# Optimization experiments

Hardware: AMD Instinct MI355X
Metric: run time of the kernel (lower is better)

## Reference

```python
import jax, jax.numpy as jnp
import numpy as np

C = 2.0 + 1e-6
_nodes, _weights = np.polynomial.laguerre.laggauss(2)
QUAD_NODES = jnp.asarray(np.maximum(_nodes, 0.01) / C, dtype=jnp.float32)
QUAD_WEIGHTS = jnp.asarray(np.maximum(_weights, 0.01) / C, dtype=jnp.float32)
H, HD, P, M = 4, 64, 16, 32  # heads, head_dim, poly_dim, num_features
NUM_LABELS = 131072


def safe_normalize(x, axis=-1, eps=1e-4):
    n = jnp.linalg.norm(x, axis=axis, keepdims=True)
    return x / jnp.maximum(n, eps)


def safe_log(x, eps=1e-8):
    return jnp.log(jnp.maximum(x, eps))


def slay_features(x, omega, anchors):
    # x: [N, H*HD]; omega: [R,H,HD,M] (pre-scaled); anchors: [P,HD] (unit-norm)
    N = x.shape[0]
    xr = safe_normalize(x.reshape(N, H, HD), axis=-1)
    poly_proj = jnp.clip(jnp.einsum('nhd,pd->nhp', xr, anchors), -1.0, 1.0)
    poly_feat = poly_proj ** 2 / np.float32(np.sqrt(P))          # [N,H,P]
    prf_proj = jnp.einsum('nhd,rhdm->rnhm', xr, omega)           # [R,N,H,M]
    s = jnp.maximum(QUAD_NODES, 1e-6).reshape(-1, 1, 1, 1)
    exp_arg = jnp.clip(prf_proj * jnp.sqrt(2.0 * s) - s, -20.0, 20.0)
    prf_feat = jnp.exp(exp_arg) / np.float32(np.sqrt(M + 1e-6))
    prf_feat = prf_feat * jnp.sqrt(jnp.maximum(QUAD_WEIGHTS, 1e-6)).reshape(-1, 1, 1, 1)
    # fuse poly x prf, concat over quadrature nodes r (r-major feature order)
    fused = poly_feat[None, :, :, :, None] * prf_feat[:, :, :, None, :]  # [R,N,H,P,M]
    return fused.transpose(1, 0, 2, 3, 4).reshape(N, -1)         # [N, R*H*P*M]


def setup_inputs() -> dict:
    key = jax.random.key(0)
    ks = jax.random.split(key, 9)
    B, L, K = 1024, 128, 8
    return {
        'indices': jax.random.randint(ks[0], (B, L), 0, 100000),
        'mask': jnp.ones((B, L), dtype=jnp.float32),
        'labels': jax.random.randint(ks[1], (B, K), 0, NUM_LABELS),
        'label_mask': jnp.ones((B, K), dtype=jnp.float32),
        'neg_indices': jax.random.randint(ks[2], (2048,), 0, NUM_LABELS),
        'embed_table': jax.random.normal(ks[3], (100000, 256), dtype=jnp.float32),
        'kernel': jax.random.normal(ks[4], (256, NUM_LABELS), dtype=jnp.float32),
        'omega': jax.random.normal(ks[5], (2, H, HD, M), dtype=jnp.float32),
        'anchors': jax.random.normal(ks[6], (P, HD), dtype=jnp.float32),
    }


def reference(indices, mask, labels, label_mask, neg_indices, embed_table, kernel, omega, anchors):
    B, K = labels.shape
    # init-time parameter normalizations from the module
    omega_n = omega / np.float32(np.sqrt(HD))
    anchors_n = anchors / jnp.linalg.norm(anchors, axis=-1, keepdims=True)
    # MeanEmbedding encoder
    embeds = embed_table[indices]                                 # [B,L,D]
    summed = jnp.sum(embeds * mask[:, :, None], axis=1)
    query = summed / jnp.maximum(jnp.sum(mask, axis=1, keepdims=True), 1.0)
    query = safe_normalize(query, axis=-1)
    phi_query = slay_features(query, omega_n, anchors_n)          # [B,F]
    # sampled classifier rows
    W = safe_normalize(kernel.T, axis=-1)                         # [num_labels,D]
    safe_labels = jnp.maximum(labels, 0)
    all_needed = jnp.concatenate([safe_labels.reshape(-1), neg_indices])  # [B*K+Nneg]
    W_subset = W[all_needed]
    phi_W = slay_features(W_subset, omega_n, anchors_n)           # [B*K+Nneg,F]
    scores = phi_query @ phi_W.T                                  # [B, B*K+Nneg]
    idx_offsets = jnp.arange(B)[:, None] * K + jnp.arange(K)[None, :]
    pos_scores = jnp.take_along_axis(scores, idx_offsets, axis=1) # [B,K]
    neg_scores = scores[:, B * K:]                                # [B,Nneg]
    all_scores = jnp.concatenate([pos_scores, neg_scores], axis=1) + 1e-8
    log_Z = jax.scipy.special.logsumexp(safe_log(all_scores), axis=1)
    log_probs = safe_log(pos_scores + 1e-8) - log_Z[:, None]
    return -jnp.sum(log_probs * label_mask) / (jnp.sum(label_mask) + 1e-6)
```

## Files before the change

kernel.cpp:

```cpp
#include <hip/hip_runtime.h>
#include <math.h>

#define B_Q 1024
#define L_SEQ 128
#define D_EMB 256
#define NLAB 131072
#define LBL_ROWS 8192
#define NEG_ROWS 2048
#define W_ROWS 10240
#define CROW 320
#define LST 82
#define RPB 8

__device__ __forceinline__ float wave_sum(float v) {
#pragma unroll
  for (int off = 32; off > 0; off >>= 1) v += __shfl_xor(v, off, 64);
  return v;
}

__device__ __forceinline__ void slay_tail(const float* __restrict__ sx, int t,
                                          const float* __restrict__ anchT,
                                          const float* __restrict__ omega,
                                          float* __restrict__ outrow) {
  if (t < 64) {
    const int h = t >> 4, p = t & 15;
    const float* x = sx + h * 64;
    float d = 0.f;
#pragma unroll
    for (int dd = 0; dd < 64; dd++) d = fmaf(x[dd], anchT[dd * 16 + p], d);
    d = fminf(fmaxf(d, -1.0f), 1.0f);
    outrow[h * 16 + p] = d * d * 0.25f;
  }
  {
    const int r = t >> 7, h = (t >> 5) & 3;
    const float* x = sx + h * 64;
    const float* om = omega + (size_t)(t >> 5) * 2048 + (t & 31);
    float d = 0.f;
#pragma unroll
    for (int dd = 0; dd < 64; dd++) d = fmaf(x[dd], om[dd * 32], d);
    const float proj = d * 0.125f;
    const float s = r ? 1.70710592763316f : 0.29289307236691f;
    const float w = r ? 0.07322326809171f : 0.42677648190829f;
    float arg = proj * sqrtf(2.0f * s) - s;
    arg = fminf(fmaxf(arg, -20.0f), 20.0f);
    outrow[64 + t] = expf(arg) * (sqrtf(w) / sqrtf(32.000001f));
  }
}

__global__ __launch_bounds__(256) void k_prep(const float* __restrict__ anchors,
                                              float* __restrict__ anchT,
                                              float* __restrict__ negparts,
                                              int* __restrict__ hist) {
  const int t = threadIdx.x, bx = blockIdx.x;
  if (bx == 0) {
    if (t < 64) {
      for (int p = 0; p < 16; p++) {
        const float v = anchors[p * 64 + t];
        const float n = sqrtf(wave_sum(v * v));
        anchT[t * 16 + p] = v / n;
      }
    }
  } else if (bx <= 256) {
    negparts[(bx - 1) * 256 + t] = 0.f;
  } else {
    hist[(bx - 257) * 256 + t] = 0;
  }
}

__global__ __launch_bounds__(256) void k_mark(const int* __restrict__ labels,
                                              const int* __restrict__ negidx,
                                              int* __restrict__ jidx,
                                              int* __restrict__ hist) {
  const int i = blockIdx.x * 256 + threadIdx.x;
  if (i >= W_ROWS) return;
  int j;
  if (i < LBL_ROWS) { j = labels[i]; if (j < 0) j = 0; }
  else               { j = negidx[i - LBL_ROWS]; }
  jidx[i] = j;
  atomicAdd(&hist[j >> 6], 1);
}

__global__ __launch_bounds__(256) void k_scan(int* __restrict__ hist) {
  __shared__ int s[256];
  const int t = threadIdx.x;
  int v[8]; int sum = 0;
#pragma unroll
  for (int e = 0; e < 8; e++) { v[e] = hist[t * 8 + e]; sum += v[e]; }
  s[t] = sum; __syncthreads();
  for (int off = 1; off < 256; off <<= 1) {
    const int x = s[t];
    const int y = (t >= off) ? s[t - off] : 0;
    __syncthreads();
    s[t] = x + y;
    __syncthreads();
  }
  int run = s[t] - sum;
#pragma unroll
  for (int e = 0; e < 8; e++) { hist[t * 8 + e] = run; run += v[e]; }
}

__global__ __launch_bounds__(256) void k_scatter(const int* __restrict__ jidx,
                                                 int* __restrict__ hist,
                                                 int* __restrict__ sorted) {
  const int i = blockIdx.x * 256 + threadIdx.x;
  if (i >= W_ROWS) return;
  const int pos = atomicAdd(&hist[jidx[i] >> 6], 1);
  sorted[pos] = i;
}

__global__ __launch_bounds__(256) void k_query(const int* __restrict__ indices,
                                               const float* __restrict__ mask,
                                               const float* __restrict__ embed,
                                               const float* __restrict__ anchT,
                                               const float* __restrict__ omega,
                                               float* __restrict__ qcomp) {
  const int b = blockIdx.x, t = threadIdx.x;
  const int wv = t >> 6, ln = t & 63;
  __shared__ int sidx[L_SEQ];
  __shared__ float smask[L_SEQ];
  __shared__ float4 spart[256];
  __shared__ float smsum[4];
  __shared__ float sx[256];
  if (t < L_SEQ) { sidx[t] = indices[b * L_SEQ + t]; smask[t] = mask[b * L_SEQ + t]; }
  __syncthreads();
  float4 acc = {0.f, 0.f, 0.f, 0.f};
  float msum = 0.f;
#pragma unroll 8
  for (int l = wv * 32; l < wv * 32 + 32; l++) {
    const float m = smask[l];
    msum += m;
    const float4 e = *(const float4*)(embed + (size_t)sidx[l] * D_EMB + ln * 4);
    acc.x = fmaf(e.x, m, acc.x); acc.y = fmaf(e.y, m, acc.y);
    acc.z = fmaf(e.z, m, acc.z); acc.w = fmaf(e.w, m, acc.w);
  }
  spart[wv * 64 + ln] = acc;
  if (ln == 0) smsum[wv] = msum;
  __syncthreads();
  const float* spf = (const float*)spart;
  float q = spf[t] + spf[256 + t] + spf[512 + t] + spf[768 + t];
  const float mt = smsum[0] + smsum[1] + smsum[2] + smsum[3];
  q /= fmaxf(mt, 1.0f);
  const float ss = wave_sum(q * q);
  sx[t] = q / fmaxf(sqrtf(ss), 1e-4f);
  __syncthreads();
  slay_tail(sx, t, anchT, omega, qcomp + (size_t)b * CROW);
}

__global__ __launch_bounds__(256) void k_wrows(const int* __restrict__ sorted,
                                               const int* __restrict__ jidx,
                                               const float* __restrict__ kern,
                                               const float* __restrict__ anchT,
                                               const float* __restrict__ omega,
                                               float* __restrict__ wcomp) {
  __shared__ int sj[RPB];
  __shared__ int ssid[RPB];
  __shared__ float sx[RPB * 256];
  __shared__ float snorm[RPB * 4];
  const int tid = threadIdx.x;
  const int cb = (blockIdx.x & 7) * 160 + (blockIdx.x >> 3);
  const int i0 = cb * RPB;

  if (tid < RPB) {
    const int sid = sorted[i0 + tid];
    ssid[tid] = sid;
    sj[tid] = jidx[sid];
  }
  __syncthreads();

#pragma unroll
  for (int k = 0; k < RPB; k++) {
    const int idx = k * 256 + tid;
    sx[idx] = kern[(size_t)(idx & 255) * NLAB + sj[idx >> 8]];
  }
  __syncthreads();

  {
    const int row = tid >> 5, sub = tid & 31;
    const float* xp = sx + row * 256 + sub * 8;
    float ssum = 0.f;
#pragma unroll
    for (int e = 0; e < 8; e++) ssum = fmaf(xp[e], xp[e], ssum);
    ssum += __shfl_xor(ssum, 1, 64);
    ssum += __shfl_xor(ssum, 2, 64);
    ssum += __shfl_xor(ssum, 4, 64);
    if ((sub & 7) == 0) snorm[row * 4 + (sub >> 3)] = fmaxf(sqrtf(ssum), 1e-4f);
  }
  __syncthreads();
#pragma unroll
  for (int k = 0; k < RPB; k++) {
    const int idx = k * 256 + tid;
    sx[idx] /= snorm[(idx >> 8) * 4 + ((idx >> 6) & 3)];
  }
  __syncthreads();

  {
    const int h = (tid >> 5) & 3, r = tid >> 7;
    const float* om = omega + (size_t)(tid >> 5) * 2048 + (tid & 31);
    float acc[RPB];
#pragma unroll
    for (int row = 0; row < RPB; row++) acc[row] = 0.f;
#pragma unroll
    for (int dd = 0; dd < 64; dd += 2) {
      const float o0 = om[dd * 32], o1 = om[dd * 32 + 32];
#pragma unroll
      for (int row = 0; row < RPB; row++) {
        const float2 xv = *(const float2*)(sx + row * 256 + h * 64 + dd);
        acc[row] = fmaf(xv.x, o0, fmaf(xv.y, o1, acc[row]));
      }
    }
    const float s = r ? 1.70710592763316f : 0.29289307236691f;
    const float w = r ? 0.07322326809171f : 0.42677648190829f;
    const float sc = sqrtf(2.0f * s);
    const float outs = sqrtf(w) / sqrtf(32.000001f);
#pragma unroll
    for (int row = 0; row < RPB; row++) {
      float arg = acc[row] * 0.125f * sc - s;
      arg = fminf(fmaxf(arg, -20.0f), 20.0f);
      wcomp[(size_t)ssid[row] * CROW + 64 + tid] = expf(arg) * outs;
    }
  }

  {
    const int hp = tid & 63, rp = tid >> 6;
    const int h = hp >> 4, p = hp & 15;
    const float* x0 = sx + (rp * 2) * 256 + h * 64;
    const float* x1 = x0 + 256;
    float d0 = 0.f, d1 = 0.f;
#pragma unroll
    for (int dd = 0; dd < 64; dd++) {
      const float a = anchT[dd * 16 + p];
      d0 = fmaf(x0[dd], a, d0);
      d1 = fmaf(x1[dd], a, d1);
    }
    d0 = fminf(fmaxf(d0, -1.0f), 1.0f);
    d1 = fminf(fmaxf(d1, -1.0f), 1.0f);
    wcomp[(size_t)ssid[rp * 2] * CROW + h * 16 + p]     = d0 * d0 * 0.25f;
    wcomp[(size_t)ssid[rp * 2 + 1] * CROW + h * 16 + p] = d1 * d1 * 0.25f;
  }
}

__global__ __launch_bounds__(128) void k_neg(const float* __restrict__ qcomp,
                                             const float* __restrict__ wcomp,
                                             float* __restrict__ negparts) {
  __shared__ float qt[64 * LST];
  __shared__ float wt[32 * LST];
  const int tid = threadIdx.x;
  const int qb0 = blockIdx.x * 64;
  const int wr0 = LBL_ROWS + blockIdx.y * 32;
  const int h = blockIdx.z;

  for (int idx = tid; idx < 96 * 20; idx += 128) {
    const int row = idx / 20, c4 = idx % 20;
    int col, lcol;
    if (c4 < 4)       { col = h * 16 + c4 * 4;              lcol = c4 * 4; }
    else if (c4 < 12) { col = 64 + h * 32 + (c4 - 4) * 4;   lcol = 16 + (c4 - 4) * 4; }
    else              { col = 192 + h * 32 + (c4 - 12) * 4; lcol = 48 + (c4 - 12) * 4; }
    const bool isq = row < 64;
    const int grow = isq ? (qb0 + row) : (wr0 + row - 64);
    const float4 v = *(const float4*)((isq ? qcomp : wcomp) + (size_t)grow * CROW + col);
    float* dst = (isq ? qt + row * LST : wt + (row - 64) * LST) + lcol;
    dst[0] = v.x; dst[1] = v.y; dst[2] = v.z; dst[3] = v.w;
  }
  __syncthreads();

  const int qg = tid >> 3;
  const int wg = tid & 7;
  const float* qb = qt + (qg * 4) * LST;
  const float* wb = wt + (wg * 4) * LST;

  float pd[4][4] = {{0.f}}, pf[4][4] = {{0.f}};
#pragma unroll
  for (int kc = 0; kc < 8; kc++) {
    float2 qv[4], wv[4];
#pragma unroll
    for (int i = 0; i < 4; i++) qv[i] = *(const float2*)(qb + i * LST + 2 * kc);
#pragma unroll
    for (int j = 0; j < 4; j++) wv[j] = *(const float2*)(wb + j * LST + 2 * kc);
#pragma unroll
    for (int i = 0; i < 4; i++)
#pragma unroll
      for (int j = 0; j < 4; j++) {
        pd[i][j] = fmaf(qv[i].x, wv[j].x, pd[i][j]);
        pd[i][j] = fmaf(qv[i].y, wv[j].y, pd[i][j]);
      }
  }
#pragma unroll 8
  for (int kc = 0; kc < 32; kc++) {
    float2 qv[4], wv[4];
#pragma unroll
    for (int i = 0; i < 4; i++) qv[i] = *(const float2*)(qb + i * LST + 16 + 2 * kc);
#pragma unroll
    for (int j = 0; j < 4; j++) wv[j] = *(const float2*)(wb + j * LST + 16 + 2 * kc);
#pragma unroll
    for (int i = 0; i < 4; i++)
#pragma unroll
      for (int j = 0; j < 4; j++) {
        pf[i][j] = fmaf(qv[i].x, wv[j].x, pf[i][j]);
        pf[i][j] = fmaf(qv[i].y, wv[j].y, pf[i][j]);
      }
  }

#pragma unroll
  for (int i = 0; i < 4; i++) {
    float acc = 0.f;
#pragma unroll
    for (int j = 0; j < 4; j++) acc += pd[i][j] * pf[i][j];
#pragma unroll
    for (int off = 1; off < 8; off <<= 1) acc += __shfl_xor(acc, off, 64);
    if (wg == 0) atomicAdd(&negparts[blockIdx.y * B_Q + qb0 + qg * 4 + i], acc);
  }
}

__global__ __launch_bounds__(256) void k_pos(const float* __restrict__ qcomp,
                                             const float* __restrict__ wcomp,
                                             float* __restrict__ pos) {
  const int tid = threadIdx.x;
  const int g = blockIdx.x * 64 + (tid >> 2);
  const int h = tid & 3;
  const float* q = qcomp + (size_t)(g >> 3) * CROW;
  const float* w = wcomp + (size_t)g * CROW;
  float pd = 0.f, pf = 0.f;
#pragma unroll
  for (int c = 0; c < 4; c++) {
    const float4 qv = *(const float4*)(q + h * 16 + c * 4);
    const float4 wv = *(const float4*)(w + h * 16 + c * 4);
    pd += qv.x * wv.x + qv.y * wv.y + qv.z * wv.z + qv.w * wv.w;
  }
#pragma unroll
  for (int r = 0; r < 2; r++)
#pragma unroll
    for (int c = 0; c < 8; c++) {
      const float4 qv = *(const float4*)(q + 64 + r * 128 + h * 32 + c * 4);
      const float4 wv = *(const float4*)(w + 64 + r * 128 + h * 32 + c * 4);
      pf += qv.x * wv.x + qv.y * wv.y + qv.z * wv.z + qv.w * wv.w;
    }
  float sc = pd * pf;
  sc += __shfl_xor(sc, 1, 64);
  sc += __shfl_xor(sc, 2, 64);
  if (h == 0) pos[g] = sc;
}

__global__ __launch_bounds__(1024) void k_loss(const float* __restrict__ pos,
                                               const float* __restrict__ negparts,
                                               const float* __restrict__ lmask,
                                               float* __restrict__ out) {
  const int b = threadIdx.x;
  float lp[8];
  float possum = 0.f;
#pragma unroll
  for (int k = 0; k < 8; k++) { lp[k] = pos[b * 8 + k]; possum += lp[k]; }
  float negsum = 0.f;
#pragma unroll 8
  for (int c = 0; c < 64; c++) negsum += negparts[c * B_Q + b];
  const float Z = possum + negsum + 2.056e-5f;
  const float logZ = logf(Z);
  float local = 0.f, lsum = 0.f;
#pragma unroll
  for (int k = 0; k < 8; k++) {
    const float lm = lmask[b * 8 + k];
    local += lm * (logf(lp[k] + 1e-8f) - logZ);
    lsum += lm;
  }
  local = wave_sum(local);
  lsum = wave_sum(lsum);
  __shared__ float r1[16], r2[16];
  const int wid = b >> 6;
  if ((b & 63) == 0) { r1[wid] = local; r2[wid] = lsum; }
  __syncthreads();
  if (b == 0) {
    float t1 = 0.f, t2 = 0.f;
    for (int wv = 0; wv < 16; wv++) { t1 += r1[wv]; t2 += r2[wv]; }
    out[0] = -t1 / (t2 + 1e-6f);
  }
}

extern "C" void kernel_launch(void* const* d_in, const int* in_sizes, int n_in,
                              void* d_out, int out_size, void* d_ws, size_t ws_size,
                              hipStream_t stream) {
  const int* indices  = (const int*)d_in[0];
  const float* mask   = (const float*)d_in[1];
  const int* labels   = (const int*)d_in[2];
  const float* lmask  = (const float*)d_in[3];
  const int* negidx   = (const int*)d_in[4];
  const float* embed  = (const float*)d_in[5];
  const float* kern   = (const float*)d_in[6];
  const float* omega  = (const float*)d_in[7];
  const float* anchors= (const float*)d_in[8];
  float* out = (float*)d_out;

  float* ws = (float*)d_ws;
  float* anchT    = ws;
  float* qcomp    = anchT + 1024;
  float* wcomp    = qcomp + (size_t)B_Q * CROW;
  float* pos      = wcomp + (size_t)W_ROWS * CROW;
  float* negparts = pos + LBL_ROWS;
  int*   jidx     = (int*)(negparts + 64 * B_Q);
  int*   sorted   = jidx + W_ROWS;
  int*   hist     = sorted + W_ROWS;

  k_prep<<<265, 256, 0, stream>>>(anchors, anchT, negparts, hist);
  k_mark<<<40, 256, 0, stream>>>(labels, negidx, jidx, hist);
  k_scan<<<1, 256, 0, stream>>>(hist);
  k_scatter<<<40, 256, 0, stream>>>(jidx, hist, sorted);
  k_query<<<B_Q, 256, 0, stream>>>(indices, mask, embed, anchT, omega, qcomp);
  k_wrows<<<W_ROWS / RPB, 256, 0, stream>>>(sorted, jidx, kern, anchT, omega, wcomp);
  k_neg<<<dim3(16, 64, 4), 128, 0, stream>>>(qcomp, wcomp, negparts);
  k_pos<<<128, 256, 0, stream>>>(qcomp, wcomp, pos);
  k_loss<<<1, 1024, 0, stream>>>(pos, negparts, lmask, out);
}
```

Baseline: 357.6 us.

## Fuse nine launches into four: single-block sort, merged feature and score kernels

Combines the anchor prep, histogram marking, scan and scatter into one setup kernel. The histogram work is done in shared memory by a single block instead of global atomics spread over three launches. The query-feature and W-row feature kernels become one grid split by block index, and the negative and positive scoring kernels likewise share one launch. The aim is to cut launch gaps and let independent stages overlap on the GPU. In exchange the whole sort runs serially in one block, and both fused kernels now take the larger shared-memory footprint of the two paths.

```diff
diff --git a/kernel.cpp b/kernel.cpp
--- a/kernel.cpp
+++ b/kernel.cpp
@@ -32,7 +32,8 @@
     outrow[h * 16 + p] = d * d * 0.25f;
   }
   {
-    const int r = t >> 7, h = (t >> 5) & 3;
+    const int r = t >> 7;
+    const int h = (t >> 5) & 3;
     const float* x = sx + h * 64;
     const float* om = omega + (size_t)(t >> 5) * 2048 + (t & 31);
     float d = 0.f;
@@ -47,10 +48,15 @@
   }
 }
 
-__global__ __launch_bounds__(256) void k_prep(const float* __restrict__ anchors,
-                                              float* __restrict__ anchT,
-                                              float* __restrict__ negparts,
-                                              int* __restrict__ hist) {
+__global__ __launch_bounds__(256) void k_setup(const float* __restrict__ anchors,
+                                               const int* __restrict__ labels,
+                                               const int* __restrict__ negidx,
+                                               float* __restrict__ anchT,
+                                               float* __restrict__ negparts,
+                                               int* __restrict__ jidx,
+                                               int* __restrict__ sorted) {
+  __shared__ int shist[2048];
+  __shared__ int s2[256];
   const int t = threadIdx.x, bx = blockIdx.x;
   if (bx == 0) {
     if (t < 64) {
@@ -63,281 +69,270 @@
   } else if (bx <= 256) {
     negparts[(bx - 1) * 256 + t] = 0.f;
   } else {
-    hist[(bx - 257) * 256 + t] = 0;
-  }
-}
-
-__global__ __launch_bounds__(256) void k_mark(const int* __restrict__ labels,
-                                              const int* __restrict__ negidx,
-                                              int* __restrict__ jidx,
-                                              int* __restrict__ hist) {
-  const int i = blockIdx.x * 256 + threadIdx.x;
-  if (i >= W_ROWS) return;
-  int j;
-  if (i < LBL_ROWS) { j = labels[i]; if (j < 0) j = 0; }
-  else               { j = negidx[i - LBL_ROWS]; }
-  jidx[i] = j;
-  atomicAdd(&hist[j >> 6], 1);
-}
-
-__global__ __launch_bounds__(256) void k_scan(int* __restrict__ hist) {
-  __shared__ int s[256];
-  const int t = threadIdx.x;
-  int v[8]; int sum = 0;
-#pragma unroll
-  for (int e = 0; e < 8; e++) { v[e] = hist[t * 8 + e]; sum += v[e]; }
-  s[t] = sum; __syncthreads();
-  for (int off = 1; off < 256; off <<= 1) {
-    const int x = s[t];
-    const int y = (t >= off) ? s[t - off] : 0;
-    __syncthreads();
-    s[t] = x + y;
-    __syncthreads();
-  }
-  int run = s[t] - sum;
-#pragma unroll
-  for (int e = 0; e < 8; e++) { hist[t * 8 + e] = run; run += v[e]; }
-}
-
-__global__ __launch_bounds__(256) void k_scatter(const int* __restrict__ jidx,
-                                                 int* __restrict__ hist,
-                                                 int* __restrict__ sorted) {
-  const int i = blockIdx.x * 256 + threadIdx.x;
-  if (i >= W_ROWS) return;
-  const int pos = atomicAdd(&hist[jidx[i] >> 6], 1);
-  sorted[pos] = i;
-}
-
-__global__ __launch_bounds__(256) void k_query(const int* __restrict__ indices,
-                                               const float* __restrict__ mask,
-                                               const float* __restrict__ embed,
-                                               const float* __restrict__ anchT,
-                                               const float* __restrict__ omega,
-                                               float* __restrict__ qcomp) {
-  const int b = blockIdx.x, t = threadIdx.x;
-  const int wv = t >> 6, ln = t & 63;
-  __shared__ int sidx[L_SEQ];
-  __shared__ float smask[L_SEQ];
-  __shared__ float4 spart[256];
-  __shared__ float smsum[4];
-  __shared__ float sx[256];
-  if (t < L_SEQ) { sidx[t] = indices[b * L_SEQ + t]; smask[t] = mask[b * L_SEQ + t]; }
-  __syncthreads();
-  float4 acc = {0.f, 0.f, 0.f, 0.f};
-  float msum = 0.f;
+    for (int i = t; i < 2048; i += 256) shist[i] = 0;
+    __syncthreads();
+    for (int i = t; i < W_ROWS; i += 256) {
+      int j;
+      if (i < LBL_ROWS) { j = labels[i]; if (j < 0) j = 0; }
+      else               { j = negidx[i - LBL_ROWS]; }
+      jidx[i] = j;
+      atomicAdd(&shist[j >> 6], 1);
+    }
+    __syncthreads();
+    int v[8]; int sum = 0;
+#pragma unroll
+    for (int e = 0; e < 8; e++) { v[e] = shist[t * 8 + e]; sum += v[e]; }
+    s2[t] = sum; __syncthreads();
+    for (int off = 1; off < 256; off <<= 1) {
+      const int x = s2[t];
+      const int y = (t >= off) ? s2[t - off] : 0;
+      __syncthreads();
+      s2[t] = x + y;
+      __syncthreads();
+    }
+    int run = s2[t] - sum;
+#pragma unroll
+    for (int e = 0; e < 8; e++) { shist[t * 8 + e] = run; run += v[e]; }
+    __syncthreads();
+    for (int i = t; i < W_ROWS; i += 256) {
+      const int p = atomicAdd(&shist[jidx[i] >> 6], 1);
+      sorted[p] = i;
+    }
+  }
+}
+
+__global__ __launch_bounds__(256) void k_feat(const int* __restrict__ indices,
+                                              const float* __restrict__ mask,
+                                              const float* __restrict__ embed,
+                                              const float* __restrict__ kern,
+                                              const float* __restrict__ anchT,
+                                              const float* __restrict__ omega,
+                                              const int* __restrict__ jidx,
+                                              const int* __restrict__ sorted,
+                                              float* __restrict__ qcomp,
+                                              float* __restrict__ wcomp) {
+  __shared__ __align__(16) float smem[2112];
+  const int tid = threadIdx.x;
+
+  if (blockIdx.x < B_Q) {
+    const int b = blockIdx.x, t = tid;
+    const int wv = t >> 6, ln = t & 63;
+    int* sidx = (int*)smem;
+    float* smask = smem + 128;
+    float4* spart = (float4*)(smem + 256);
+    float* smsum = smem + 1280;
+    float* sx = smem + 1296;
+    if (t < L_SEQ) { sidx[t] = indices[b * L_SEQ + t]; smask[t] = mask[b * L_SEQ + t]; }
+    __syncthreads();
+    float4 acc = {0.f, 0.f, 0.f, 0.f};
+    float msum = 0.f;
 #pragma unroll 8
-  for (int l = wv * 32; l < wv * 32 + 32; l++) {
-    const float m = smask[l];
-    msum += m;
-    const float4 e = *(const float4*)(embed + (size_t)sidx[l] * D_EMB + ln * 4);
-    acc.x = fmaf(e.x, m, acc.x); acc.y = fmaf(e.y, m, acc.y);
-    acc.z = fmaf(e.z, m, acc.z); acc.w = fmaf(e.w, m, acc.w);
-  }
-  spart[wv * 64 + ln] = acc;
-  if (ln == 0) smsum[wv] = msum;
-  __syncthreads();
-  const float* spf = (const float*)spart;
-  float q = spf[t] + spf[256 + t] + spf[512 + t] + spf[768 + t];
-  const float mt = smsum[0] + smsum[1] + smsum[2] + smsum[3];
-  q /= fmaxf(mt, 1.0f);
-  const float ss = wave_sum(q * q);
-  sx[t] = q / fmaxf(sqrtf(ss), 1e-4f);
-  __syncthreads();
-  slay_tail(sx, t, anchT, omega, qcomp + (size_t)b * CROW);
-}
-
-__global__ __launch_bounds__(256) void k_wrows(const int* __restrict__ sorted,
-                                               const int* __restrict__ jidx,
-                                               const float* __restrict__ kern,
-                                               const float* __restrict__ anchT,
-                                               const float* __restrict__ omega,
-                                               float* __restrict__ wcomp) {
-  __shared__ int sj[RPB];
-  __shared__ int ssid[RPB];
-  __shared__ float sx[RPB * 256];
-  __shared__ float snorm[RPB * 4];
-  const int tid = threadIdx.x;
-  const int cb = (blockIdx.x & 7) * 160 + (blockIdx.x >> 3);
-  const int i0 = cb * RPB;
-
-  if (tid < RPB) {
-    const int sid = sorted[i0 + tid];
-    ssid[tid] = sid;
-    sj[tid] = jidx[sid];
-  }
-  __syncthreads();
-
-#pragma unroll
-  for (int k = 0; k < RPB; k++) {
-    const int idx = k * 256 + tid;
-    sx[idx] = kern[(size_t)(idx & 255) * NLAB + sj[idx >> 8]];
-  }
-  __syncthreads();
-
-  {
-    const int row = tid >> 5, sub = tid & 31;
-    const float* xp = sx + row * 256 + sub * 8;
-    float ssum = 0.f;
-#pragma unroll
-    for (int e = 0; e < 8; e++) ssum = fmaf(xp[e], xp[e], ssum);
-    ssum += __shfl_xor(ssum, 1, 64);
-    ssum += __shfl_xor(ssum, 2, 64);
-    ssum += __shfl_xor(ssum, 4, 64);
-    if ((sub & 7) == 0) snorm[row * 4 + (sub >> 3)] = fmaxf(sqrtf(ssum), 1e-4f);
-  }
-  __syncthreads();
-#pragma unroll
-  for (int k = 0; k < RPB; k++) {
-    const int idx = k * 256 + tid;
-    sx[idx] /= snorm[(idx >> 8) * 4 + ((idx >> 6) & 3)];
-  }
-  __syncthreads();
-
-  {
-    const int h = (tid >> 5) & 3, r = tid >> 7;
-    const float* om = omega + (size_t)(tid >> 5) * 2048 + (tid & 31);
-    float acc[RPB];
-#pragma unroll
-    for (int row = 0; row < RPB; row++) acc[row] = 0.f;
-#pragma unroll
-    for (int dd = 0; dd < 64; dd += 2) {
-      const float o0 = om[dd * 32], o1 = om[dd * 32 + 32];
+    for (int l = wv * 32; l < wv * 32 + 32; l++) {
+      const float m = smask[l];
+      msum += m;
+      const float4 e = *(const float4*)(embed + (size_t)sidx[l] * D_EMB + ln * 4);
+      acc.x = fmaf(e.x, m, acc.x); acc.y = fmaf(e.y, m, acc.y);
+      acc.z = fmaf(e.z, m, acc.z); acc.w = fmaf(e.w, m, acc.w);
+    }
+    spart[wv * 64 + ln] = acc;
+    if (ln == 0) smsum[wv] = msum;
+    __syncthreads();
+    const float* spf = (const float*)spart;
+    float q = spf[t] + spf[256 + t] + spf[512 + t] + spf[768 + t];
+    const float mt = smsum[0] + smsum[1] + smsum[2] + smsum[3];
+    q /= fmaxf(mt, 1.0f);
+    const float ss = wave_sum(q * q);
+    sx[t] = q / fmaxf(sqrtf(ss), 1e-4f);
+    __syncthreads();
+    slay_tail(sx, t, anchT, omega, qcomp + (size_t)b * CROW);
+  } else {
+    const int lb = blockIdx.x - B_Q;
+    int* sj = (int*)smem;
+    int* ssid = (int*)smem + 8;
+    float* snorm = smem + 16;
+    float* sx = smem + 48;
+    const int cb = (lb & 7) * 160 + (lb >> 3);
+    const int i0 = cb * RPB;
+
+    if (tid < RPB) {
+      const int sid = sorted[i0 + tid];
+      ssid[tid] = sid;
+      sj[tid] = jidx[sid];
+    }
+    __syncthreads();
+
+#pragma unroll
+    for (int k = 0; k < RPB; k++) {
+      const int idx = k * 256 + tid;
+      sx[idx] = kern[(size_t)(idx & 255) * NLAB + sj[idx >> 8]];
+    }
+    __syncthreads();
+
+    {
+      const int row = tid >> 5, sub = tid & 31;
+      const float* xp = sx + row * 256 + sub * 8;
+      float ssum = 0.f;
+#pragma unroll
+      for (int e = 0; e < 8; e++) ssum = fmaf(xp[e], xp[e], ssum);
+      ssum += __shfl_xor(ssum, 1, 64);
+      ssum += __shfl_xor(ssum, 2, 64);
+      ssum += __shfl_xor(ssum, 4, 64);
+      if ((sub & 7) == 0) snorm[row * 4 + (sub >> 3)] = fmaxf(sqrtf(ssum), 1e-4f);
+    }
+    __syncthreads();
+#pragma unroll
+    for (int k = 0; k < RPB; k++) {
+      const int idx = k * 256 + tid;
+      sx[idx] /= snorm[(idx >> 8) * 4 + ((idx >> 6) & 3)];
+    }
+    __syncthreads();
+
+    {
+      const int h = (tid >> 5) & 3, r = tid >> 7;
+      const float* om = omega + (size_t)(tid >> 5) * 2048 + (tid & 31);
+      float acc[RPB];
+#pragma unroll
+      for (int row = 0; row < RPB; row++) acc[row] = 0.f;
+#pragma unroll
+      for (int dd = 0; dd < 64; dd += 2) {
+        const float o0 = om[dd * 32], o1 = om[dd * 32 + 32];
+#pragma unroll
+        for (int row = 0; row < RPB; row++) {
+          const float2 xv = *(const float2*)(sx + row * 256 + h * 64 + dd);
+          acc[row] = fmaf(xv.x, o0, fmaf(xv.y, o1, acc[row]));
+        }
+      }
+      const float s = r ? 1.70710592763316f : 0.29289307236691f;
+      const float w = r ? 0.07322326809171f : 0.42677648190829f;
+      const float sc = sqrtf(2.0f * s);
+      const float outs = sqrtf(w) / sqrtf(32.000001f);
 #pragma unroll
       for (int row = 0; row < RPB; row++) {
-        const float2 xv = *(const float2*)(sx + row * 256 + h * 64 + dd);
-        acc[row] = fmaf(xv.x, o0, fmaf(xv.y, o1, acc[row]));
+        float arg = acc[row] * 0.125f * sc - s;
+        arg = fminf(fmaxf(arg, -20.0f), 20.0f);
+        wcomp[(size_t)ssid[row] * CROW + 64 + tid] = expf(arg) * outs;
       }
     }
-    const float s = r ? 1.70710592763316f : 0.29289307236691f;
-    const float w = r ? 0.07322326809171f : 0.42677648190829f;
-    const float sc = sqrtf(2.0f * s);
-    const float outs = sqrtf(w) / sqrtf(32.000001f);
-#pragma unroll
-    for (int row = 0; row < RPB; row++) {
-      float arg = acc[row] * 0.125f * sc - s;
-      arg = fminf(fmaxf(arg, -20.0f), 20.0f);
-      wcomp[(size_t)ssid[row] * CROW + 64 + tid] = expf(arg) * outs;
-    }
-  }
-
-  {
-    const int hp = tid & 63, rp = tid >> 6;
-    const int h = hp >> 4, p = hp & 15;
-    const float* x0 = sx + (rp * 2) * 256 + h * 64;
-    const float* x1 = x0 + 256;
-    float d0 = 0.f, d1 = 0.f;
-#pragma unroll
-    for (int dd = 0; dd < 64; dd++) {
-      const float a = anchT[dd * 16 + p];
-      d0 = fmaf(x0[dd], a, d0);
-      d1 = fmaf(x1[dd], a, d1);
-    }
-    d0 = fminf(fmaxf(d0, -1.0f), 1.0f);
-    d1 = fminf(fmaxf(d1, -1.0f), 1.0f);
-    wcomp[(size_t)ssid[rp * 2] * CROW + h * 16 + p]     = d0 * d0 * 0.25f;
-    wcomp[(size_t)ssid[rp * 2 + 1] * CROW + h * 16 + p] = d1 * d1 * 0.25f;
-  }
-}
-
-__global__ __launch_bounds__(128) void k_neg(const float* __restrict__ qcomp,
-                                             const float* __restrict__ wcomp,
-                                             float* __restrict__ negparts) {
+
+    {
+      const int hp = tid & 63, rp = tid >> 6;
+      const int h = hp >> 4, p = hp & 15;
+      const float* x0 = sx + (rp * 2) * 256 + h * 64;
+      const float* x1 = x0 + 256;
+      float d0 = 0.f, d1 = 0.f;
+#pragma unroll
+      for (int dd = 0; dd < 64; dd++) {
+        const float a = anchT[dd * 16 + p];
+        d0 = fmaf(x0[dd], a, d0);
+        d1 = fmaf(x1[dd], a, d1);
+      }
+      d0 = fminf(fmaxf(d0, -1.0f), 1.0f);
+      d1 = fminf(fmaxf(d1, -1.0f), 1.0f);
+      wcomp[(size_t)ssid[rp * 2] * CROW + h * 16 + p]     = d0 * d0 * 0.25f;
+      wcomp[(size_t)ssid[rp * 2 + 1] * CROW + h * 16 + p] = d1 * d1 * 0.25f;
+    }
+  }
+}
+
+__global__ __launch_bounds__(128) void k_score(const float* __restrict__ qcomp,
+                                               const float* __restrict__ wcomp,
+                                               float* __restrict__ negparts,
+                                               float* __restrict__ pos) {
   __shared__ float qt[64 * LST];
   __shared__ float wt[32 * LST];
   const int tid = threadIdx.x;
-  const int qb0 = blockIdx.x * 64;
-  const int wr0 = LBL_ROWS + blockIdx.y * 32;
-  const int h = blockIdx.z;
-
-  for (int idx = tid; idx < 96 * 20; idx += 128) {
-    const int row = idx / 20, c4 = idx % 20;
-    int col, lcol;
-    if (c4 < 4)       { col = h * 16 + c4 * 4;              lcol = c4 * 4; }
-    else if (c4 < 12) { col = 64 + h * 32 + (c4 - 4) * 4;   lcol = 16 + (c4 - 4) * 4; }
-    else              { col = 192 + h * 32 + (c4 - 12) * 4; lcol = 48 + (c4 - 12) * 4; }
-    const bool isq = row < 64;
-    const int grow = isq ? (qb0 + row) : (wr0 + row - 64);
-    const float4 v = *(const float4*)((isq ? qcomp : wcomp) + (size_t)grow * CROW + col);
-    float* dst = (isq ? qt + row * LST : wt + (row - 64) * LST) + lcol;
-    dst[0] = v.x; dst[1] = v.y; dst[2] = v.z; dst[3] = v.w;
-  }
-  __syncthreads();
-
-  const int qg = tid >> 3;
-  const int wg = tid & 7;
-  const float* qb = qt + (qg * 4) * LST;
-  const float* wb = wt + (wg * 4) * LST;
-
-  float pd[4][4] = {{0.f}}, pf[4][4] = {{0.f}};
-#pragma unroll
-  for (int kc = 0; kc < 8; kc++) {
-    float2 qv[4], wv[4];
-#pragma unroll
-    for (int i = 0; i < 4; i++) qv[i] = *(const float2*)(qb + i * LST + 2 * kc);
-#pragma unroll
-    for (int j = 0; j < 4; j++) wv[j] = *(const float2*)(wb + j * LST + 2 * kc);
-#pragma unroll
-    for (int i = 0; i < 4; i++)
-#pragma unroll
-      for (int j = 0; j < 4; j++) {
-        pd[i][j] = fmaf(qv[i].x, wv[j].x, pd[i][j]);
-        pd[i][j] = fmaf(qv[i].y, wv[j].y, pd[i][j]);
+
+  if (blockIdx.x < 4096) {
+    const int qb0 = (blockIdx.x & 15) * 64;
+    const int wb  = (blockIdx.x >> 4) & 63;
+    const int wr0 = LBL_ROWS + wb * 32;
+    const int h   = blockIdx.x >> 10;
+
+    for (int idx = tid; idx < 96 * 20; idx += 128) {
+      const int row = idx / 20, c4 = idx % 20;
+      int col, lcol;
+      if (c4 < 4)       { col = h * 16 + c4 * 4;              lcol = c4 * 4; }
+      else if (c4 < 12) { col = 64 + h * 32 + (c4 - 4) * 4;   lcol = 16 + (c4 - 4) * 4; }
+      else              { col = 192 + h * 32 + (c4 - 12) * 4; lcol = 48 + (c4 - 12) * 4; }
+      const bool isq = row < 64;
+      const int grow = isq ? (qb0 + row) : (wr0 + row - 64);
+      const float4 v = *(const float4*)((isq ? qcomp : wcomp) + (size_t)grow * CROW + col);
+      float* dst = (isq ? qt + row * LST : wt + (row - 64) * LST) + lcol;
+      dst[0] = v.x; dst[1] = v.y; dst[2] = v.z; dst[3] = v.w;
+    }
+    __syncthreads();
+
+    const int qg = tid >> 3;
+    const int wg = tid & 7;
+    const float* qb = qt + (qg * 4) * LST;
+    const float* wbp = wt + (wg * 4) * LST;
+
+    float pd[4][4] = {{0.f}}, pf[4][4] = {{0.f}};
+#pragma unroll
+    for (int kc = 0; kc < 8; kc++) {
+      float2 qv[4], wv[4];
+#pragma unroll
+      for (int i = 0; i < 4; i++) qv[i] = *(const float2*)(qb + i * LST + 2 * kc);
+#pragma unroll
+      for (int j = 0; j < 4; j++) wv[j] = *(const float2*)(wbp + j * LST + 2 * kc);
+#pragma unroll
+      for (int i = 0; i < 4; i++)
+#pragma unroll
+        for (int j = 0; j < 4; j++) {
+          pd[i][j] = fmaf(qv[i].x, wv[j].x, pd[i][j]);
+          pd[i][j] = fmaf(qv[i].y, wv[j].y, pd[i][j]);
+        }
+    }
+#pragma unroll 8
+    for (int kc = 0; kc < 32; kc++) {
+      float2 qv[4], wv[4];
+#pragma unroll
+      for (int i = 0; i < 4; i++) qv[i] = *(const float2*)(qb + i * LST + 16 + 2 * kc);
+#pragma unroll
+      for (int j = 0; j < 4; j++) wv[j] = *(const float2*)(wbp + j * LST + 16 + 2 * kc);
+#pragma unroll
+      for (int i = 0; i < 4; i++)
+#pragma unroll
+        for (int j = 0; j < 4; j++) {
+          pf[i][j] = fmaf(qv[i].x, wv[j].x, pf[i][j]);
+          pf[i][j] = fmaf(qv[i].y, wv[j].y, pf[i][j]);
+        }
+    }
+
+#pragma unroll
+    for (int i = 0; i < 4; i++) {
+      float acc = 0.f;
+#pragma unroll
+      for (int j = 0; j < 4; j++) acc += pd[i][j] * pf[i][j];
+#pragma unroll
+      for (int off = 1; off < 8; off <<= 1) acc += __shfl_xor(acc, off, 64);
+      if (wg == 0) atomicAdd(&negparts[wb * B_Q + qb0 + qg * 4 + i], acc);
+    }
+  } else {
+    const int g = (blockIdx.x - 4096) * 32 + (tid >> 2);
+    const int h = tid & 3;
+    const float* q = qcomp + (size_t)(g >> 3) * CROW;
+    const float* w = wcomp + (size_t)g * CROW;
+    float pd = 0.f, pf = 0.f;
+#pragma unroll
+    for (int c = 0; c < 4; c++) {
+      const float4 qv = *(const float4*)(q + h * 16 + c * 4);
+      const float4 wv = *(const float4*)(w + h * 16 + c * 4);
+      pd += qv.x * wv.x + qv.y * wv.y + qv.z * wv.z + qv.w * wv.w;
+    }
+#pragma unroll
+    for (int r = 0; r < 2; r++)
+#pragma unroll
+      for (int c = 0; c < 8; c++) {
+        const float4 qv = *(const float4*)(q + 64 + r * 128 + h * 32 + c * 4);
+        const float4 wv = *(const float4*)(w + 64 + r * 128 + h * 32 + c * 4);
+        pf += qv.x * wv.x + qv.y * wv.y + qv.z * wv.z + qv.w * wv.w;
       }
-  }
-#pragma unroll 8
-  for (int kc = 0; kc < 32; kc++) {
-    float2 qv[4], wv[4];
-#pragma unroll
-    for (int i = 0; i < 4; i++) qv[i] = *(const float2*)(qb + i * LST + 16 + 2 * kc);
-#pragma unroll
-    for (int j = 0; j < 4; j++) wv[j] = *(const float2*)(wb + j * LST + 16 + 2 * kc);
-#pragma unroll
-    for (int i = 0; i < 4; i++)
-#pragma unroll
-      for (int j = 0; j < 4; j++) {
-        pf[i][j] = fmaf(qv[i].x, wv[j].x, pf[i][j]);
-        pf[i][j] = fmaf(qv[i].y, wv[j].y, pf[i][j]);
-      }
-  }
-
-#pragma unroll
-  for (int i = 0; i < 4; i++) {
-    float acc = 0.f;
-#pragma unroll
-    for (int j = 0; j < 4; j++) acc += pd[i][j] * pf[i][j];
-#pragma unroll
-    for (int off = 1; off < 8; off <<= 1) acc += __shfl_xor(acc, off, 64);
-    if (wg == 0) atomicAdd(&negparts[blockIdx.y * B_Q + qb0 + qg * 4 + i], acc);
-  }
-}
-
-__global__ __launch_bounds__(256) void k_pos(const float* __restrict__ qcomp,
-                                             const float* __restrict__ wcomp,
-                                             float* __restrict__ pos) {
-  const int tid = threadIdx.x;
-  const int g = blockIdx.x * 64 + (tid >> 2);
-  const int h = tid & 3;
-  const float* q = qcomp + (size_t)(g >> 3) * CROW;
-  const float* w = wcomp + (size_t)g * CROW;
-  float pd = 0.f, pf = 0.f;
-#pragma unroll
-  for (int c = 0; c < 4; c++) {
-    const float4 qv = *(const float4*)(q + h * 16 + c * 4);
-    const float4 wv = *(const float4*)(w + h * 16 + c * 4);
-    pd += qv.x * wv.x + qv.y * wv.y + qv.z * wv.z + qv.w * wv.w;
-  }
-#pragma unroll
-  for (int r = 0; r < 2; r++)
-#pragma unroll
-    for (int c = 0; c < 8; c++) {
-      const float4 qv = *(const float4*)(q + 64 + r * 128 + h * 32 + c * 4);
-      const float4 wv = *(const float4*)(w + 64 + r * 128 + h * 32 + c * 4);
-      pf += qv.x * wv.x + qv.y * wv.y + qv.z * wv.z + qv.w * wv.w;
-    }
-  float sc = pd * pf;
-  sc += __shfl_xor(sc, 1, 64);
-  sc += __shfl_xor(sc, 2, 64);
-  if (h == 0) pos[g] = sc;
+    float sc = pd * pf;
+    sc += __shfl_xor(sc, 1, 64);
+    sc += __shfl_xor(sc, 2, 64);
+    if (h == 0) pos[g] = sc;
+  }
 }
 
 __global__ __launch_bounds__(1024) void k_loss(const float* __restrict__ pos,
@@ -396,15 +391,10 @@
   float* negparts = pos + LBL_ROWS;
   int*   jidx     = (int*)(negparts + 64 * B_Q);
   int*   sorted   = jidx + W_ROWS;
-  int*   hist     = sorted + W_ROWS;
-
-  k_prep<<<265, 256, 0, stream>>>(anchors, anchT, negparts, hist);
-  k_mark<<<40, 256, 0, stream>>>(labels, negidx, jidx, hist);
-  k_scan<<<1, 256, 0, stream>>>(hist);
-  k_scatter<<<40, 256, 0, stream>>>(jidx, hist, sorted);
-  k_query<<<B_Q, 256, 0, stream>>>(indices, mask, embed, anchT, omega, qcomp);
-  k_wrows<<<W_ROWS / RPB, 256, 0, stream>>>(sorted, jidx, kern, anchT, omega, wcomp);
-  k_neg<<<dim3(16, 64, 4), 128, 0, stream>>>(qcomp, wcomp, negparts);
-  k_pos<<<128, 256, 0, stream>>>(qcomp, wcomp, pos);
+
+  k_setup<<<258, 256, 0, stream>>>(anchors, labels, negidx, anchT, negparts, jidx, sorted);
+  k_feat<<<B_Q + W_ROWS / RPB, 256, 0, stream>>>(indices, mask, embed, kern, anchT, omega,
+                                                 jidx, sorted, qcomp, wcomp);
+  k_score<<<4096 + 256, 128, 0, stream>>>(qcomp, wcomp, negparts, pos);
   k_loss<<<1, 1024, 0, stream>>>(pos, negparts, lmask, out);
 }
```

After: 370.1 us. 3.5% more time.
